# Kernel tuning notes

Hardware: AMD Instinct MI355X
Metric: run time of the kernel (lower is better)

## Reference

```python
import jax, jax.numpy as jnp
import numpy as np

D = 1024
H = 16
DK = D // H
SCALE = 1.0 / jnp.sqrt(jnp.float32(DK))


def setup_inputs() -> dict:
    key0 = jax.random.key(0)
    ks = jax.random.split(key0, 11)
    B, S = 2, 2048
    std = 1.0 / np.sqrt(D)
    inp = {
        "query": jax.random.normal(ks[0], (B, S, D), jnp.float32),
        "key": jax.random.normal(ks[1], (B, S, D), jnp.float32),
        "value": jax.random.normal(ks[2], (B, S, D), jnp.float32),
        "wq": jax.random.normal(ks[3], (D, D), jnp.float32) * std,
        "bq": jax.random.normal(ks[4], (D,), jnp.float32) * std,
        "wk": jax.random.normal(ks[5], (D, D), jnp.float32) * std,
        "bk": jax.random.normal(ks[6], (D,), jnp.float32) * std,
        "wv": jax.random.normal(ks[7], (D, D), jnp.float32) * std,
        "bv": jax.random.normal(ks[8], (D,), jnp.float32) * std,
        "wo": jax.random.normal(ks[9], (D, D), jnp.float32) * std,
        "bo": jax.random.normal(ks[10], (D,), jnp.float32) * std,
    }
    return inp


def _split_heads(x):
    # [B,S,D] -> [B,H,S,dk]
    B, S, _ = x.shape
    return x.reshape(B, S, H, DK).transpose(0, 2, 1, 3)


def reference(query, key, value, wq, bq, wk, bk, wv, bv, wo, bo):
    B, S, _ = query.shape
    # Linear projections (torch nn.Linear: x @ W^T + b)
    q = _split_heads(query @ wq.T + bq)
    k = _split_heads(key @ wk.T + bk)
    v = _split_heads(value @ wv.T + bv)
    # Scaled dot-product attention scores [B,H,S,S]
    scores = jnp.einsum("bhqd,bhkd->bhqk", q * SCALE, k)
    attention = jax.nn.softmax(scores, axis=-1)
    # Dropout in eval mode == identity
    out = jnp.einsum("bhqk,bhkd->bhqd", attention, v)
    out = out.transpose(0, 2, 1, 3).reshape(B, S, D)
    out = out @ wo.T + bo
    return out, attention
```

## Files before the change

### kernel.cpp

```cpp
#include <hip/hip_runtime.h>
#include <stdint.h>

typedef __attribute__((ext_vector_type(4))) float f32x4;
typedef __attribute__((ext_vector_type(8))) short short8;

#define MFMA16(a, b, c) __builtin_amdgcn_mfma_f32_16x16x32_bf16((a), (b), (c), 0, 0, 0)
#define EXP2(x) __builtin_amdgcn_exp2f(x)
#define LOG2(x) __builtin_amdgcn_logf(x)

__device__ __forceinline__ unsigned short f2bf(float f) {
  unsigned int x = __float_as_uint(f);
  return (unsigned short)((x + 0x7fffu + ((x >> 16) & 1u)) >> 16);
}

__device__ __forceinline__ unsigned int cvtpk(float lo, float hi) {
  unsigned int d;
  asm("v_cvt_pk_bf16_f32 %0, %1, %2" : "=v"(d) : "v"(lo), "v"(hi));
  return d;
}

__device__ __forceinline__ void gl2lds16(const void* g, void* l) {
  __builtin_amdgcn_global_load_lds((const __attribute__((address_space(1))) void*)g,
                                   (__attribute__((address_space(3))) void*)l, 16, 0, 0);
}

__device__ __forceinline__ void load8cv(const float* __restrict__ s, void* d) {
  const f32x4* p = (const f32x4*)s;
  f32x4 a = p[0], b = p[1];
  short8 t;
  t[0] = (short)f2bf(a[0]); t[1] = (short)f2bf(a[1]);
  t[2] = (short)f2bf(a[2]); t[3] = (short)f2bf(a[3]);
  t[4] = (short)f2bf(b[0]); t[5] = (short)f2bf(b[1]);
  t[6] = (short)f2bf(b[2]); t[7] = (short)f2bf(b[3]);
  *(short8*)d = t;
}

#define ENT_V0 asm volatile("s_waitcnt vmcnt(0)\ns_barrier" ::: "memory")
#define ENT_V4 asm volatile("s_waitcnt vmcnt(4)\ns_barrier" ::: "memory")

__global__ __launch_bounds__(256) void cast_all(const float* __restrict__ wq,
                                                const float* __restrict__ wk,
                                                const float* __restrict__ wv,
                                                const float* __restrict__ wo,
                                                const float* __restrict__ q_in,
                                                const float* __restrict__ k_in,
                                                const float* __restrict__ v_in,
                                                unsigned short* __restrict__ W16,
                                                unsigned short* __restrict__ Qin,
                                                unsigned short* __restrict__ Kin,
                                                unsigned short* __restrict__ Vin) {
  int i = blockIdx.x * 256 + threadIdx.x;
  if (i < 524288) {
    int which = i >> 17;
    int off = (i & 131071) * 8;
    const float* src = which == 0 ? wq : which == 1 ? wk : which == 2 ? wv : wo;
    load8cv(src + off, W16 + (size_t)which * 1048576 + off);
  } else {
    int j = i - 524288;
    int which = j >> 19;
    int off = (j & 524287) * 8;
    const float* src = which == 0 ? q_in : which == 1 ? k_in : v_in;
    unsigned short* dst = which == 0 ? Qin : which == 1 ? Kin : Vin;
    load8cv(src + off, dst + off);
  }
}

__global__ __launch_bounds__(256) void qkv_proj(const unsigned short* __restrict__ Qin,
                                                const unsigned short* __restrict__ Kin,
                                                const unsigned short* __restrict__ Vin,
                                                const unsigned short* __restrict__ W16,
                                                const float* __restrict__ bq,
                                                const float* __restrict__ bk,
                                                const float* __restrict__ bv,
                                                unsigned short* __restrict__ Q16,
                                                unsigned short* __restrict__ K16,
                                                unsigned short* __restrict__ V16) {
  const int z = blockIdx.z;
  const unsigned short* A = z == 0 ? Qin : z == 1 ? Kin : Vin;
  const unsigned short* Bt = W16 + (size_t)z * 1048576;
  const float* bias = z == 0 ? bq : z == 1 ? bk : bv;
  unsigned short* C = z == 0 ? Q16 : z == 1 ? K16 : V16;
  const float oscale = z == 0 ? 0.18033688f : 1.0f;
  const int K = 1024, N = 1024;

  __shared__ __align__(16) char lds[32768];
  char* As = lds;
  char* Bs = lds + 16384;
  const int tid = threadIdx.x;
  const int lane = tid & 63;
  const int wv = tid >> 6;
  const int g = lane >> 4, r = lane & 15;
  const int wm = wv >> 1, wn = wv & 1;
  const int m0 = blockIdx.y * 128, n0 = blockIdx.x * 128;

  f32x4 acc[4][4];
#pragma unroll
  for (int m = 0; m < 4; ++m)
#pragma unroll
    for (int n = 0; n < 4; ++n) acc[m][n] = (f32x4){0.f, 0.f, 0.f, 0.f};

  for (int k0 = 0; k0 < K; k0 += 64) {
    __syncthreads();
#pragma unroll
    for (int i = 0; i < 4; ++i) {
      int c = (wv * 4 + i) * 64 + lane;
      int row = c >> 3;
      gl2lds16(Bt + (size_t)(n0 + row) * K + k0 + (c & 7) * 8, Bs + (wv * 4 + i) * 1024);
    }
#pragma unroll
    for (int i = 0; i < 4; ++i) {
      int c = (wv * 4 + i) * 64 + lane;
      int row = c >> 3;
      gl2lds16(A + (size_t)(m0 + row) * K + k0 + (c & 7) * 8, As + (wv * 4 + i) * 1024);
    }
    __syncthreads();
#pragma unroll
    for (int kk = 0; kk < 2; ++kk) {
      short8 af[4], bfr[4];
#pragma unroll
      for (int m = 0; m < 4; ++m)
        af[m] = *(const short8*)(As + (wm * 64 + m * 16 + r) * 128 + kk * 64 + g * 16);
#pragma unroll
      for (int n = 0; n < 4; ++n)
        bfr[n] = *(const short8*)(Bs + (wn * 64 + n * 16 + r) * 128 + kk * 64 + g * 16);
#pragma unroll
      for (int m = 0; m < 4; ++m)
#pragma unroll
        for (int n = 0; n < 4; ++n) acc[m][n] = MFMA16(af[m], bfr[n], acc[m][n]);
    }
  }

#pragma unroll
  for (int n = 0; n < 4; ++n) {
    int col = n0 + wn * 64 + n * 16 + r;
    float bv_ = bias[col];
#pragma unroll
    for (int m = 0; m < 4; ++m)
#pragma unroll
      for (int i = 0; i < 4; ++i) {
        int rowg = m0 + wm * 64 + m * 16 + 4 * g + i;
        C[(size_t)rowg * N + col] = f2bf((acc[m][n][i] + bv_) * oscale);
      }
  }
}

__global__ __launch_bounds__(256) void o_proj(const unsigned short* __restrict__ A,
                                              const unsigned short* __restrict__ Bt,
                                              const float* __restrict__ bias,
                                              float* __restrict__ C) {
  const int K = 1024, N = 1024;
  __shared__ __align__(16) char lds[24576];
  char* As = lds;
  char* Bs = lds + 16384;
  const int tid = threadIdx.x;
  const int lane = tid & 63;
  const int wv = tid >> 6;
  const int g = lane >> 4, r = lane & 15;
  const int wm = wv >> 1, wn = wv & 1;
  const int m0 = blockIdx.y * 128, n0 = blockIdx.x * 64;

  f32x4 acc[4][2];
#pragma unroll
  for (int m = 0; m < 4; ++m)
#pragma unroll
    for (int n = 0; n < 2; ++n) acc[m][n] = (f32x4){0.f, 0.f, 0.f, 0.f};

  for (int k0 = 0; k0 < K; k0 += 64) {
    __syncthreads();
#pragma unroll
    for (int i = 0; i < 2; ++i) {
      int c = (wv * 2 + i) * 64 + lane;
      int row = c >> 3;
      gl2lds16(Bt + (size_t)(n0 + row) * K + k0 + (c & 7) * 8, Bs + (wv * 2 + i) * 1024);
    }
#pragma unroll
    for (int i = 0; i < 4; ++i) {
      int c = (wv * 4 + i) * 64 + lane;
      int row = c >> 3;
      gl2lds16(A + (size_t)(m0 + row) * K + k0 + (c & 7) * 8, As + (wv * 4 + i) * 1024);
    }
    __syncthreads();
#pragma unroll
    for (int kk = 0; kk < 2; ++kk) {
      short8 af[4], bfr[2];
#pragma unroll
      for (int m = 0; m < 4; ++m)
        af[m] = *(const short8*)(As + (wm * 64 + m * 16 + r) * 128 + kk * 64 + g * 16);
#pragma unroll
      for (int n = 0; n < 2; ++n)
        bfr[n] = *(const short8*)(Bs + (wn * 32 + n * 16 + r) * 128 + kk * 64 + g * 16);
#pragma unroll
      for (int m = 0; m < 4; ++m)
#pragma unroll
        for (int n = 0; n < 2; ++n) acc[m][n] = MFMA16(af[m], bfr[n], acc[m][n]);
    }
  }

#pragma unroll
  for (int n = 0; n < 2; ++n) {
    int col = n0 + wn * 32 + n * 16 + r;
    float bv_ = bias[col];
#pragma unroll
    for (int m = 0; m < 4; ++m)
#pragma unroll
      for (int i = 0; i < 4; ++i) {
        int rowg = m0 + wm * 64 + m * 16 + 4 * g + i;
        C[(size_t)rowg * N + col] = acc[m][n][i] + bv_;
      }
  }
}

__global__ __launch_bounds__(256) void transpose_v(const unsigned short* __restrict__ V,
                                                   unsigned short* __restrict__ Vt) {
  int t = blockIdx.x * 256 + threadIdx.x;
  int d = t & 63;
  int sc = (t >> 6) & 255;
  int bh = t >> 14;
  int b = bh >> 4, h = bh & 15;
  unsigned short vals[8];
#pragma unroll
  for (int j = 0; j < 8; ++j)
    vals[j] = V[(size_t)(b * 2048 + sc * 8 + j) * 1024 + h * 64 + d];
  *(short8*)&Vt[((size_t)bh * 64 + d) * 2048 + sc * 8] = *(short8*)vals;
}

__global__ __launch_bounds__(256, 4) void attn_fused(const unsigned short* __restrict__ Q,
                                                     const unsigned short* __restrict__ K,
                                                     const unsigned short* __restrict__ Vt,
                                                     float* __restrict__ attn,
                                                     unsigned short* __restrict__ O) {
  __shared__ __align__(16) char lds[32768];
  const int tid = threadIdx.x;
  const int lane = tid & 63;
  const int wv = tid >> 6;
  const int g = lane >> 4, r = lane & 15;
  int nb = (blockIdx.x & 7) * 128 + (blockIdx.x >> 3);
  const int qt = nb & 31, bh = nb >> 5, h = bh & 15, b = bh >> 4;
  const int qloc = qt * 64 + wv * 16;
  const int qrow0 = b * 2048 + qloc;
  const unsigned short* Kbh = K + (size_t)b * 2048 * 1024 + h * 64;
  const unsigned short* Vbh = Vt + (size_t)bh * 64 * 2048;
  float* attn_bh = attn + (size_t)bh * 2048 * 2048;

  short8 qf[2];
#pragma unroll
  for (int kk = 0; kk < 2; ++kk)
    qf[kk] = *(const short8*)&Q[(size_t)(qrow0 + r) * 1024 + h * 64 + kk * 32 + g * 8];

#define P1_ISSUE(bb, ktt)                                                      \
  do {                                                                         \
    _Pragma("unroll") for (int i_ = 0; i_ < 4; ++i_) {                         \
      int c_ = (wv * 4 + i_) * 64 + lane;                                      \
      int kr_ = c_ >> 3;                                                       \
      int scb_ = ((c_ & 7) * 16) ^ ((kr_ & 7) << 4);                           \
      gl2lds16(Kbh + (size_t)((ktt) + kr_) * 1024 + (scb_ >> 1),               \
               (bb) + (wv * 4 + i_) * 1024);                                   \
    }                                                                          \
  } while (0)
#define P2_ISSUE(bb, ktt)                                                      \
  do {                                                                         \
    _Pragma("unroll") for (int i_ = 0; i_ < 4; ++i_) {                         \
      int c_ = (wv * 4 + i_) * 64 + lane;                                      \
      int kr_ = (c_ >> 3) & 63;                                                \
      int scb_ = ((c_ & 7) * 16) ^ ((kr_ & 7) << 4);                           \
      const unsigned short* src_ =                                             \
          (c_ < 512) ? (Kbh + (size_t)((ktt) + kr_) * 1024 + (scb_ >> 1))      \
                     : (Vbh + (size_t)kr_ * 2048 + (ktt) + (scb_ >> 1));       \
      gl2lds16(src_, (bb) + (wv * 4 + i_) * 1024);                             \
    }                                                                          \
  } while (0)

  float lrow = 0.f;
  int cur = 0;
  P1_ISSUE(lds, 0);
  for (int t = 0; t < 16; ++t) {
    char* bcur = lds + (cur << 14);
    ENT_V0;
    if (t < 15) P1_ISSUE(lds + ((cur ^ 1) << 14), (t + 1) * 128);
#pragma unroll
    for (int ct = 0; ct < 8; ++ct) {
      int row = ct * 16 + r;
      int sw = (row & 7) << 4;
      short8 kf0 = *(const short8*)(bcur + ((row * 128 + g * 16) ^ sw));
      short8 kf1 = *(const short8*)(bcur + ((row * 128 + 64 + g * 16) ^ sw));
      f32x4 s = (f32x4){0.f, 0.f, 0.f, 0.f};
      s = MFMA16(kf0, qf[0], s);
      s = MFMA16(kf1, qf[1], s);
      lrow += (EXP2(s[0]) + EXP2(s[1])) + (EXP2(s[2]) + EXP2(s[3]));
    }
    cur ^= 1;
  }
  lrow += __shfl_xor(lrow, 16);
  lrow += __shfl_xor(lrow, 32);
  const float negml = -LOG2(lrow);
  const f32x4 cinit = (f32x4){negml, negml, negml, negml};

  f32x4 oacc[4];
#pragma unroll
  for (int i = 0; i < 4; ++i) oacc[i] = (f32x4){0.f, 0.f, 0.f, 0.f};

  float* arow = attn_bh + (size_t)(qloc + r) * 2048 + 4 * g;
  cur = 0;
  P2_ISSUE(lds, 0);
  for (int t = 0; t < 32; ++t) {
    char* bcur = lds + (cur << 14);
    int kt = t * 64;
    if (t == 0) {
      ENT_V0;
    } else {
      ENT_V4;
    }
    if (t < 31) P2_ISSUE(lds + ((cur ^ 1) << 14), kt + 64);
    unsigned w[4][2];
#pragma unroll
    for (int ct = 0; ct < 4; ++ct) {
      int row = ct * 16 + r;
      int sw = (row & 7) << 4;
      short8 kf0 = *(const short8*)(bcur + ((row * 128 + g * 16) ^ sw));
      short8 kf1 = *(const short8*)(bcur + ((row * 128 + 64 + g * 16) ^ sw));
      f32x4 s = MFMA16(kf0, qf[0], cinit);
      s = MFMA16(kf1, qf[1], s);
      f32x4 p;
      p[0] = EXP2(s[0]); p[1] = EXP2(s[1]);
      p[2] = EXP2(s[2]); p[3] = EXP2(s[3]);
      __builtin_nontemporal_store(p, (f32x4*)(arow + kt + 16 * ct));
      w[ct][0] = cvtpk(p[0], p[1]);
      w[ct][1] = cvtpk(p[2], p[3]);
    }
    __builtin_amdgcn_s_setprio(1);
#pragma unroll
    for (int kk2 = 0; kk2 < 2; ++kk2) {
      unsigned x0 = w[2 * kk2][0], y0 = w[2 * kk2 + 1][0];
      unsigned x1 = w[2 * kk2][1], y1 = w[2 * kk2 + 1][1];
      asm("v_permlane32_swap_b32 %0, %1" : "+v"(x0), "+v"(y0));
      asm("v_permlane16_swap_b32 %0, %1" : "+v"(x0), "+v"(y0));
      asm("v_permlane32_swap_b32 %0, %1" : "+v"(x1), "+v"(y1));
      asm("v_permlane16_swap_b32 %0, %1" : "+v"(x1), "+v"(y1));
      union { unsigned u[4]; short8 v8; } pau;
      pau.u[0] = x0; pau.u[1] = x1; pau.u[2] = y0; pau.u[3] = y1;
      short8 pa = pau.v8;
#pragma unroll
      for (int ct2 = 0; ct2 < 4; ++ct2) {
        int vrow = ct2 * 16 + r;
        short8 vf = *(const short8*)(bcur + 8192 +
                                     ((vrow * 128 + kk2 * 64 + g * 16) ^ ((vrow & 7) << 4)));
        oacc[ct2] = MFMA16(pa, vf, oacc[ct2]);
      }
    }
    __builtin_amdgcn_s_setprio(0);
    cur ^= 1;
  }
#pragma unroll
  for (int ct2 = 0; ct2 < 4; ++ct2)
#pragma unroll
    for (int i = 0; i < 4; ++i)
      O[(size_t)(qrow0 + 4 * g + i) * 1024 + h * 64 + ct2 * 16 + r] = f2bf(oacc[ct2][i]);
#undef P1_ISSUE
#undef P2_ISSUE
}

extern "C" void kernel_launch(void* const* d_in, const int* in_sizes, int n_in,
                              void* d_out, int out_size, void* d_ws, size_t ws_size,
                              hipStream_t stream) {
  const float* q_in = (const float*)d_in[0];
  const float* k_in = (const float*)d_in[1];
  const float* v_in = (const float*)d_in[2];
  const float* wq = (const float*)d_in[3];
  const float* bq = (const float*)d_in[4];
  const float* wk = (const float*)d_in[5];
  const float* bk = (const float*)d_in[6];
  const float* wv = (const float*)d_in[7];
  const float* bv = (const float*)d_in[8];
  const float* wo = (const float*)d_in[9];
  const float* bo = (const float*)d_in[10];

  char* ws = (char*)d_ws;
  const size_t MB8 = 8ull * 1024 * 1024;
  unsigned short* W16 = (unsigned short*)(ws);
  unsigned short* Qin = (unsigned short*)(ws + MB8);
  unsigned short* Kin = (unsigned short*)(ws + 2 * MB8);
  unsigned short* Vin = (unsigned short*)(ws + 3 * MB8);
  unsigned short* Q16 = (unsigned short*)(ws + 4 * MB8);
  unsigned short* K16 = (unsigned short*)(ws + 5 * MB8);
  unsigned short* V16 = (unsigned short*)(ws + 6 * MB8);
  unsigned short* Vt  = (unsigned short*)(ws + 7 * MB8);
  unsigned short* O16 = (unsigned short*)(ws + 6 * MB8);

  float* out = (float*)d_out;
  float* attn = out + 4194304ull;

  dim3 blk(256);
  cast_all<<<dim3(8192), blk, 0, stream>>>(wq, wk, wv, wo, q_in, k_in, v_in, W16, Qin, Kin, Vin);
  qkv_proj<<<dim3(8, 32, 3), blk, 0, stream>>>(Qin, Kin, Vin, W16, bq, bk, bv, Q16, K16, V16);
  transpose_v<<<dim3(2048), blk, 0, stream>>>(V16, Vt);
  attn_fused<<<dim3(1024), blk, 0, stream>>>(Q16, K16, Vt, attn, O16);
  o_proj<<<dim3(16, 32), blk, 0, stream>>>(O16, W16 + 3145728, bo, out);
}
```

Before: 269.4 us.

## Fuse V transpose into QKV epilogue, software-pipeline attention, widen o_proj tiles

The V projection epilogue now writes its output directly in transposed per-head layout, which removes the separate transpose_v kernel and its extra pass over global memory. The attention loop is restructured so that QK^T for the next tile is computed while exp/PV of the previous tile runs. K uses a 2-slot LDS ring and V a 3-slot ring, which raises LDS use to 40 KB. o_proj tiles widen from 128x64 to 128x128, halving the grid at the cost of more registers per thread.

Result: no change. 271.3 us (+0.7%).

```diff
diff --git a/kernel.cpp b/kernel.cpp
--- a/kernel.cpp
+++ b/kernel.cpp
@@ -3,6 +3,7 @@
 
 typedef __attribute__((ext_vector_type(4))) float f32x4;
 typedef __attribute__((ext_vector_type(8))) short short8;
+typedef __attribute__((ext_vector_type(2))) unsigned int u32x2;
 
 #define MFMA16(a, b, c) __builtin_amdgcn_mfma_f32_16x16x32_bf16((a), (b), (c), 0, 0, 0)
 #define EXP2(x) __builtin_amdgcn_exp2f(x)
@@ -37,6 +38,7 @@
 
 #define ENT_V0 asm volatile("s_waitcnt vmcnt(0)\ns_barrier" ::: "memory")
 #define ENT_V4 asm volatile("s_waitcnt vmcnt(4)\ns_barrier" ::: "memory")
+#define BAR_RAW asm volatile("s_barrier" ::: "memory")
 
 __global__ __launch_bounds__(256) void cast_all(const float* __restrict__ wq,
                                                 const float* __restrict__ wk,
@@ -74,12 +76,11 @@
                                                 const float* __restrict__ bv,
                                                 unsigned short* __restrict__ Q16,
                                                 unsigned short* __restrict__ K16,
-                                                unsigned short* __restrict__ V16) {
+                                                unsigned short* __restrict__ Vt) {
   const int z = blockIdx.z;
   const unsigned short* A = z == 0 ? Qin : z == 1 ? Kin : Vin;
   const unsigned short* Bt = W16 + (size_t)z * 1048576;
   const float* bias = z == 0 ? bq : z == 1 ? bk : bv;
-  unsigned short* C = z == 0 ? Q16 : z == 1 ? K16 : V16;
   const float oscale = z == 0 ? 0.18033688f : 1.0f;
   const int K = 1024, N = 1024;
 
@@ -130,17 +131,38 @@
     }
   }
 
-#pragma unroll
-  for (int n = 0; n < 4; ++n) {
-    int col = n0 + wn * 64 + n * 16 + r;
-    float bv_ = bias[col];
-#pragma unroll
-    for (int m = 0; m < 4; ++m)
-#pragma unroll
-      for (int i = 0; i < 4; ++i) {
-        int rowg = m0 + wm * 64 + m * 16 + 4 * g + i;
-        C[(size_t)rowg * N + col] = f2bf((acc[m][n][i] + bv_) * oscale);
+  if (z == 2) {
+    const int b_ = m0 >> 11;
+    const int s0 = (m0 & 2047) + wm * 64;
+#pragma unroll
+    for (int n = 0; n < 4; ++n) {
+      int col = n0 + wn * 64 + n * 16 + r;
+      int h_ = col >> 6, d_ = col & 63;
+      float bv_ = bias[col];
+      unsigned short* vtb = Vt + ((size_t)(b_ * 16 + h_) * 64 + d_) * 2048;
+#pragma unroll
+      for (int m = 0; m < 4; ++m) {
+        int s_ = s0 + m * 16 + 4 * g;
+        u32x2 pk;
+        pk[0] = cvtpk(acc[m][n][0] + bv_, acc[m][n][1] + bv_);
+        pk[1] = cvtpk(acc[m][n][2] + bv_, acc[m][n][3] + bv_);
+        *(u32x2*)(vtb + s_) = pk;
       }
+    }
+  } else {
+    unsigned short* C = z == 0 ? Q16 : K16;
+#pragma unroll
+    for (int n = 0; n < 4; ++n) {
+      int col = n0 + wn * 64 + n * 16 + r;
+      float bv_ = bias[col];
+#pragma unroll
+      for (int m = 0; m < 4; ++m)
+#pragma unroll
+        for (int i = 0; i < 4; ++i) {
+          int rowg = m0 + wm * 64 + m * 16 + 4 * g + i;
+          C[(size_t)rowg * N + col] = f2bf((acc[m][n][i] + bv_) * oscale);
+        }
+    }
   }
 }
 
@@ -149,7 +171,7 @@
                                               const float* __restrict__ bias,
                                               float* __restrict__ C) {
   const int K = 1024, N = 1024;
-  __shared__ __align__(16) char lds[24576];
+  __shared__ __align__(16) char lds[32768];
   char* As = lds;
   char* Bs = lds + 16384;
   const int tid = threadIdx.x;
@@ -157,21 +179,21 @@
   const int wv = tid >> 6;
   const int g = lane >> 4, r = lane & 15;
   const int wm = wv >> 1, wn = wv & 1;
-  const int m0 = blockIdx.y * 128, n0 = blockIdx.x * 64;
-
-  f32x4 acc[4][2];
+  const int m0 = blockIdx.y * 128, n0 = blockIdx.x * 128;
+
+  f32x4 acc[4][4];
 #pragma unroll
   for (int m = 0; m < 4; ++m)
 #pragma unroll
-    for (int n = 0; n < 2; ++n) acc[m][n] = (f32x4){0.f, 0.f, 0.f, 0.f};
+    for (int n = 0; n < 4; ++n) acc[m][n] = (f32x4){0.f, 0.f, 0.f, 0.f};
 
   for (int k0 = 0; k0 < K; k0 += 64) {
     __syncthreads();
 #pragma unroll
-    for (int i = 0; i < 2; ++i) {
-      int c = (wv * 2 + i) * 64 + lane;
+    for (int i = 0; i < 4; ++i) {
+      int c = (wv * 4 + i) * 64 + lane;
       int row = c >> 3;
-      gl2lds16(Bt + (size_t)(n0 + row) * K + k0 + (c & 7) * 8, Bs + (wv * 2 + i) * 1024);
+      gl2lds16(Bt + (size_t)(n0 + row) * K + k0 + (c & 7) * 8, Bs + (wv * 4 + i) * 1024);
     }
 #pragma unroll
     for (int i = 0; i < 4; ++i) {
@@ -182,23 +204,23 @@
     __syncthreads();
 #pragma unroll
     for (int kk = 0; kk < 2; ++kk) {
-      short8 af[4], bfr[2];
+      short8 af[4], bfr[4];
 #pragma unroll
       for (int m = 0; m < 4; ++m)
         af[m] = *(const short8*)(As + (wm * 64 + m * 16 + r) * 128 + kk * 64 + g * 16);
 #pragma unroll
-      for (int n = 0; n < 2; ++n)
-        bfr[n] = *(const short8*)(Bs + (wn * 32 + n * 16 + r) * 128 + kk * 64 + g * 16);
+      for (int n = 0; n < 4; ++n)
+        bfr[n] = *(const short8*)(Bs + (wn * 64 + n * 16 + r) * 128 + kk * 64 + g * 16);
 #pragma unroll
       for (int m = 0; m < 4; ++m)
 #pragma unroll
-        for (int n = 0; n < 2; ++n) acc[m][n] = MFMA16(af[m], bfr[n], acc[m][n]);
-    }
-  }
-
-#pragma unroll
-  for (int n = 0; n < 2; ++n) {
-    int col = n0 + wn * 32 + n * 16 + r;
+        for (int n = 0; n < 4; ++n) acc[m][n] = MFMA16(af[m], bfr[n], acc[m][n]);
+    }
+  }
+
+#pragma unroll
+  for (int n = 0; n < 4; ++n) {
+    int col = n0 + wn * 64 + n * 16 + r;
     float bv_ = bias[col];
 #pragma unroll
     for (int m = 0; m < 4; ++m)
@@ -208,20 +230,6 @@
         C[(size_t)rowg * N + col] = acc[m][n][i] + bv_;
       }
   }
-}
-
-__global__ __launch_bounds__(256) void transpose_v(const unsigned short* __restrict__ V,
-                                                   unsigned short* __restrict__ Vt) {
-  int t = blockIdx.x * 256 + threadIdx.x;
-  int d = t & 63;
-  int sc = (t >> 6) & 255;
-  int bh = t >> 14;
-  int b = bh >> 4, h = bh & 15;
-  unsigned short vals[8];
-#pragma unroll
-  for (int j = 0; j < 8; ++j)
-    vals[j] = V[(size_t)(b * 2048 + sc * 8 + j) * 1024 + h * 64 + d];
-  *(short8*)&Vt[((size_t)bh * 64 + d) * 2048 + sc * 8] = *(short8*)vals;
 }
 
 __global__ __launch_bounds__(256, 4) void attn_fused(const unsigned short* __restrict__ Q,
@@ -229,7 +237,7 @@
                                                      const unsigned short* __restrict__ Vt,
                                                      float* __restrict__ attn,
                                                      unsigned short* __restrict__ O) {
-  __shared__ __align__(16) char lds[32768];
+  __shared__ __align__(16) char lds[40960];
   const int tid = threadIdx.x;
   const int lane = tid & 63;
   const int wv = tid >> 6;
@@ -257,17 +265,61 @@
                (bb) + (wv * 4 + i_) * 1024);                                   \
     }                                                                          \
   } while (0)
-#define P2_ISSUE(bb, ktt)                                                      \
+#define P2_ISSUE(kb, vb, ktt)                                                  \
   do {                                                                         \
     _Pragma("unroll") for (int i_ = 0; i_ < 4; ++i_) {                         \
-      int c_ = (wv * 4 + i_) * 64 + lane;                                      \
+      int ch_ = wv * 4 + i_;                                                   \
+      int c_ = ch_ * 64 + lane;                                                \
       int kr_ = (c_ >> 3) & 63;                                                \
       int scb_ = ((c_ & 7) * 16) ^ ((kr_ & 7) << 4);                           \
-      const unsigned short* src_ =                                             \
-          (c_ < 512) ? (Kbh + (size_t)((ktt) + kr_) * 1024 + (scb_ >> 1))      \
-                     : (Vbh + (size_t)kr_ * 2048 + (ktt) + (scb_ >> 1));       \
-      gl2lds16(src_, (bb) + (wv * 4 + i_) * 1024);                             \
+      if (ch_ < 8)                                                             \
+        gl2lds16(Kbh + (size_t)((ktt) + kr_) * 1024 + (scb_ >> 1),             \
+                 (kb) + ch_ * 1024);                                           \
+      else                                                                     \
+        gl2lds16(Vbh + (size_t)kr_ * 2048 + (ktt) + (scb_ >> 1),               \
+                 (vb) + (ch_ - 8) * 1024);                                     \
     }                                                                          \
+  } while (0)
+#define QKT(kb, sdst)                                                          \
+  do {                                                                         \
+    _Pragma("unroll") for (int ct = 0; ct < 4; ++ct) {                         \
+      int row = ct * 16 + r;                                                   \
+      int sw = (row & 7) << 4;                                                 \
+      short8 kf0 = *(const short8*)((kb) + ((row * 128 + g * 16) ^ sw));       \
+      short8 kf1 = *(const short8*)((kb) + ((row * 128 + 64 + g * 16) ^ sw));  \
+      f32x4 s_ = MFMA16(kf0, qf[0], cinit);                                    \
+      sdst[ct] = MFMA16(kf1, qf[1], s_);                                       \
+    }                                                                          \
+  } while (0)
+#define FINISH(vb, ktp)                                                        \
+  do {                                                                         \
+    unsigned w[4][2];                                                          \
+    _Pragma("unroll") for (int ct = 0; ct < 4; ++ct) {                         \
+      f32x4 p;                                                                 \
+      p[0] = EXP2(sprev[ct][0]); p[1] = EXP2(sprev[ct][1]);                    \
+      p[2] = EXP2(sprev[ct][2]); p[3] = EXP2(sprev[ct][3]);                    \
+      __builtin_nontemporal_store(p, (f32x4*)(arow + (ktp) + 16 * ct));        \
+      w[ct][0] = cvtpk(p[0], p[1]); w[ct][1] = cvtpk(p[2], p[3]);              \
+    }                                                                          \
+    __builtin_amdgcn_s_setprio(1);                                             \
+    _Pragma("unroll") for (int kk2 = 0; kk2 < 2; ++kk2) {                      \
+      unsigned x0 = w[2 * kk2][0], y0 = w[2 * kk2 + 1][0];                     \
+      unsigned x1 = w[2 * kk2][1], y1 = w[2 * kk2 + 1][1];                     \
+      asm("v_permlane32_swap_b32 %0, %1" : "+v"(x0), "+v"(y0));                \
+      asm("v_permlane16_swap_b32 %0, %1" : "+v"(x0), "+v"(y0));                \
+      asm("v_permlane32_swap_b32 %0, %1" : "+v"(x1), "+v"(y1));                \
+      asm("v_permlane16_swap_b32 %0, %1" : "+v"(x1), "+v"(y1));                \
+      union { unsigned u[4]; short8 v8; } pau;                                 \
+      pau.u[0] = x0; pau.u[1] = x1; pau.u[2] = y0; pau.u[3] = y1;              \
+      short8 pa = pau.v8;                                                      \
+      _Pragma("unroll") for (int ct2 = 0; ct2 < 4; ++ct2) {                    \
+        int vrow = ct2 * 16 + r;                                               \
+        short8 vf = *(const short8*)((vb) +                                    \
+            ((vrow * 128 + kk2 * 64 + g * 16) ^ ((vrow & 7) << 4)));           \
+        oacc[ct2] = MFMA16(pa, vf, oacc[ct2]);                                 \
+      }                                                                        \
+    }                                                                          \
+    __builtin_amdgcn_s_setprio(0);                                             \
   } while (0)
 
   float lrow = 0.f;
@@ -298,58 +350,36 @@
   f32x4 oacc[4];
 #pragma unroll
   for (int i = 0; i < 4; ++i) oacc[i] = (f32x4){0.f, 0.f, 0.f, 0.f};
-
   float* arow = attn_bh + (size_t)(qloc + r) * 2048 + 4 * g;
-  cur = 0;
-  P2_ISSUE(lds, 0);
-  for (int t = 0; t < 32; ++t) {
-    char* bcur = lds + (cur << 14);
-    int kt = t * 64;
-    if (t == 0) {
-      ENT_V0;
-    } else {
-      ENT_V4;
-    }
-    if (t < 31) P2_ISSUE(lds + ((cur ^ 1) << 14), kt + 64);
-    unsigned w[4][2];
-#pragma unroll
-    for (int ct = 0; ct < 4; ++ct) {
-      int row = ct * 16 + r;
-      int sw = (row & 7) << 4;
-      short8 kf0 = *(const short8*)(bcur + ((row * 128 + g * 16) ^ sw));
-      short8 kf1 = *(const short8*)(bcur + ((row * 128 + 64 + g * 16) ^ sw));
-      f32x4 s = MFMA16(kf0, qf[0], cinit);
-      s = MFMA16(kf1, qf[1], s);
-      f32x4 p;
-      p[0] = EXP2(s[0]); p[1] = EXP2(s[1]);
-      p[2] = EXP2(s[2]); p[3] = EXP2(s[3]);
-      __builtin_nontemporal_store(p, (f32x4*)(arow + kt + 16 * ct));
-      w[ct][0] = cvtpk(p[0], p[1]);
-      w[ct][1] = cvtpk(p[2], p[3]);
-    }
-    __builtin_amdgcn_s_setprio(1);
-#pragma unroll
-    for (int kk2 = 0; kk2 < 2; ++kk2) {
-      unsigned x0 = w[2 * kk2][0], y0 = w[2 * kk2 + 1][0];
-      unsigned x1 = w[2 * kk2][1], y1 = w[2 * kk2 + 1][1];
-      asm("v_permlane32_swap_b32 %0, %1" : "+v"(x0), "+v"(y0));
-      asm("v_permlane16_swap_b32 %0, %1" : "+v"(x0), "+v"(y0));
-      asm("v_permlane32_swap_b32 %0, %1" : "+v"(x1), "+v"(y1));
-      asm("v_permlane16_swap_b32 %0, %1" : "+v"(x1), "+v"(y1));
-      union { unsigned u[4]; short8 v8; } pau;
-      pau.u[0] = x0; pau.u[1] = x1; pau.u[2] = y0; pau.u[3] = y1;
-      short8 pa = pau.v8;
-#pragma unroll
-      for (int ct2 = 0; ct2 < 4; ++ct2) {
-        int vrow = ct2 * 16 + r;
-        short8 vf = *(const short8*)(bcur + 8192 +
-                                     ((vrow * 128 + kk2 * 64 + g * 16) ^ ((vrow & 7) << 4)));
-        oacc[ct2] = MFMA16(pa, vf, oacc[ct2]);
-      }
-    }
-    __builtin_amdgcn_s_setprio(0);
-    cur ^= 1;
-  }
+  char* kring = lds;
+  char* vring = lds + 16384;
+
+  f32x4 sprev[4], scur[4];
+  BAR_RAW;
+  P2_ISSUE(kring, vring, 0);
+  ENT_V0;
+  P2_ISSUE(kring + 8192, vring + 8192, 64);
+  QKT(kring, sprev);
+  ENT_V0;
+  P2_ISSUE(kring, vring + 16384, 128);
+  QKT(kring + 8192, scur);
+  FINISH(vring, 0);
+#pragma unroll
+  for (int i = 0; i < 4; ++i) sprev[i] = scur[i];
+  for (int t = 2; t < 32; ++t) {
+    char* kb = kring + (t & 1) * 8192;
+    char* vbp = vring + ((t - 1) % 3) * 8192;
+    ENT_V4;
+    if (t < 31)
+      P2_ISSUE(kring + ((t + 1) & 1) * 8192, vring + ((t + 1) % 3) * 8192, (t + 1) * 64);
+    QKT(kb, scur);
+    FINISH(vbp, (t - 1) * 64);
+#pragma unroll
+    for (int i = 0; i < 4; ++i) sprev[i] = scur[i];
+    cur = cur;
+  }
+  FINISH(vring + 8192 , 31 * 64);
+
 #pragma unroll
   for (int ct2 = 0; ct2 < 4; ++ct2)
 #pragma unroll
@@ -357,6 +387,8 @@
       O[(size_t)(qrow0 + 4 * g + i) * 1024 + h * 64 + ct2 * 16 + r] = f2bf(oacc[ct2][i]);
 #undef P1_ISSUE
 #undef P2_ISSUE
+#undef QKT
+#undef FINISH
 }
 
 extern "C" void kernel_launch(void* const* d_in, const int* in_sizes, int n_in,
@@ -382,17 +414,15 @@
   unsigned short* Vin = (unsigned short*)(ws + 3 * MB8);
   unsigned short* Q16 = (unsigned short*)(ws + 4 * MB8);
   unsigned short* K16 = (unsigned short*)(ws + 5 * MB8);
-  unsigned short* V16 = (unsigned short*)(ws + 6 * MB8);
-  unsigned short* Vt  = (unsigned short*)(ws + 7 * MB8);
-  unsigned short* O16 = (unsigned short*)(ws + 6 * MB8);
+  unsigned short* Vt  = (unsigned short*)(ws + 6 * MB8);
+  unsigned short* O16 = (unsigned short*)(ws + 7 * MB8);
 
   float* out = (float*)d_out;
   float* attn = out + 4194304ull;
 
   dim3 blk(256);
   cast_all<<<dim3(8192), blk, 0, stream>>>(wq, wk, wv, wo, q_in, k_in, v_in, W16, Qin, Kin, Vin);
-  qkv_proj<<<dim3(8, 32, 3), blk, 0, stream>>>(Qin, Kin, Vin, W16, bq, bk, bv, Q16, K16, V16);
-  transpose_v<<<dim3(2048), blk, 0, stream>>>(V16, Vt);
+  qkv_proj<<<dim3(8, 32, 3), blk, 0, stream>>>(Qin, Kin, Vin, W16, bq, bk, bv, Q16, K16, Vt);
   attn_fused<<<dim3(1024), blk, 0, stream>>>(Q16, K16, Vt, attn, O16);
-  o_proj<<<dim3(16, 32), blk, 0, stream>>>(O16, W16 + 3145728, bo, out);
-}
+  o_proj<<<dim3(8, 32), blk, 0, stream>>>(O16, W16 + 3145728, bo, out);
+}
```
